# Kernel optimization log

Measured on AMD Instinct MI355X. Metric: run time of the kernel, lower is better.

Reference implementation:

```python
import jax, jax.numpy as jnp
import numpy as np

L = 2000          # per-modality dialogue length (all_dia_len)
M = 3             # num_modal
F = 512           # feature_size
E = 400000        # number of edges (<= 500000 edge_weight params)
N = M * L         # total nodes
NUM_LAYERS = 2
EW_SIZE = 500000
W_SCALE = 0.044   # ~1/sqrt(F) to keep activations sane


def setup_inputs() -> dict:
    key = jax.random.key(0)
    ks = jax.random.split(key, 9)
    x_a = jax.random.normal(ks[0], (L, F), jnp.float32)
    x_v = jax.random.normal(ks[1], (L, F), jnp.float32)
    x_t = jax.random.normal(ks[2], (L, F), jnp.float32)
    edge_index = jax.random.randint(ks[3], (2, E), 0, N, dtype=jnp.int32)
    edge_weight_param = jnp.ones((EW_SIZE,), jnp.float32)
    gcn_W = jax.random.normal(ks[4], (NUM_LAYERS, F, F), jnp.float32) * W_SCALE
    gcn_b = jnp.zeros((NUM_LAYERS, F), jnp.float32)
    fc_W = jax.random.normal(ks[5], (NUM_LAYERS, F, F), jnp.float32) * W_SCALE
    fc_b = jnp.zeros((NUM_LAYERS, F), jnp.float32)
    return {
        "x_a": x_a, "x_v": x_v, "x_t": x_t,
        "edge_weight_param": edge_weight_param,
        "gcn_W": gcn_W, "gcn_b": gcn_b,
        "fc_W": fc_W, "fc_b": fc_b,
        "edge_index": edge_index,
    }


def _gcn_fact(edge_index, edge_weight, num_nodes):
    # sparse edge list -> dense adjacency (scatter-add, duplicate edges coalesce)
    adj = jnp.zeros((num_nodes, num_nodes), edge_weight.dtype)
    adj = adj.at[edge_index[0], edge_index[1]].add(edge_weight)
    row_sum = adj.sum(axis=1)
    # torch: pow(row_sum, -0.5), inf -> 0  (safe form for zero-degree nodes)
    pos = row_sum > 0
    d_inv_sqrt = jnp.where(pos, jax.lax.rsqrt(jnp.where(pos, row_sum, 1.0)), 0.0)
    # D^{-1/2} A D^{-1/2} via row/col broadcast (same math as diag matmuls)
    return d_inv_sqrt[:, None] * adj * d_inv_sqrt[None, :]


def reference(x_a, x_v, x_t, edge_weight_param, gcn_W, gcn_b, fc_W, fc_b, edge_index):
    feature = jnp.concatenate([x_a, x_v, x_t], axis=0)      # [N, F]
    edge_weight = edge_weight_param[: edge_index.shape[1]]   # [E]
    gcn = _gcn_fact(edge_index, edge_weight, feature.shape[0])
    feature_sum = feature
    for i in range(NUM_LAYERS):
        # encoder layer: one dense GCN propagation + projection
        feature = jax.nn.relu(gcn @ feature @ gcn_W[i] + gcn_b[i])
        # fc layer: Linear + LeakyReLU (dropout = identity at eval)
        feature_sum = feature_sum + jax.nn.leaky_relu(feature @ fc_W[i] + fc_b[i], 0.01)
    # chunk back into per-modality features
    return tuple(jnp.split(feature_sum, M, axis=0))
```

## Files before the change

### kernel.cpp

```cpp
#include <hip/hip_runtime.h>
#include <hip/hip_bf16.h>

#define LL 2000
#define MM 3
#define FF 512
#define NN (MM * LL)
#define NQ 4
#define QW 1500
#define CAPQ 64

typedef __attribute__((ext_vector_type(8))) short bf16x8;
typedef __attribute__((ext_vector_type(4))) float f32x4;

__device__ __forceinline__ unsigned short f2bf(float x) {
    __hip_bfloat16 b = __float2bfloat16(x);
    return *(unsigned short*)&b;
}

__device__ __forceinline__ void gload16(const void* gsrc, void* ldst) {
    __builtin_amdgcn_global_load_lds((const __attribute__((address_space(1))) unsigned int*)gsrc,
                                     (__attribute__((address_space(3))) unsigned int*)ldst,
                                     16, 0, 0);
}

__global__ __launch_bounds__(256) void prep(const float* __restrict__ xa,
                                            const float* __restrict__ xv,
                                            const float* __restrict__ xt,
                                            unsigned short* __restrict__ feat,
                                            float* __restrict__ out_sum,
                                            const float* __restrict__ gcnW,
                                            const float* __restrict__ fcW,
                                            unsigned short* __restrict__ Wt) {
    __shared__ unsigned short tile[64][65];
    int b = blockIdx.x;
    int tid = threadIdx.x;
    if (b < 3000) {
        int idx4 = b * 256 + tid;
        const int per4 = (LL * FF) / 4;
        const float4* src;
        int off;
        if (idx4 < per4)            { src = (const float4*)xa; off = idx4; }
        else if (idx4 < 2 * per4)   { src = (const float4*)xv; off = idx4 - per4; }
        else                        { src = (const float4*)xt; off = idx4 - 2 * per4; }
        float4 v = src[off];
        ((float4*)out_sum)[idx4] = v;
        ushort4 pk;
        pk.x = f2bf(v.x); pk.y = f2bf(v.y); pk.z = f2bf(v.z); pk.w = f2bf(v.w);
        ((ushort4*)feat)[idx4] = pk;
    } else {
        int idx = b - 3000;
        int mz = idx >> 6;
        int rem = idx & 63;
        int k0 = (rem >> 3) * 64;
        int n0 = (rem & 7) * 64;
        int layer = (mz < 2) ? mz : mz - 2;
        const float* src = (mz < 2) ? (gcnW + (size_t)layer * FF * FF)
                                    : (fcW + (size_t)layer * FF * FF);
        int slot = (mz < 2) ? (mz * 2) : ((mz - 2) * 2 + 1);
        unsigned short* dst = Wt + (size_t)slot * FF * FF;
        for (int i = tid; i < 64 * 64; i += 256) {
            int r = i >> 6, c = i & 63;
            tile[r][c] = f2bf(src[(size_t)(k0 + r) * FF + n0 + c]);
        }
        __syncthreads();
        for (int i = tid; i < 64 * 64; i += 256) {
            int r = i >> 6, c = i & 63;
            dst[(size_t)(n0 + r) * FF + k0 + c] = tile[c][r];
        }
    }
}

__global__ __launch_bounds__(256) void gemm0_scatter(const unsigned short* __restrict__ A,
                                                     const unsigned short* __restrict__ Bt,
                                                     unsigned short* __restrict__ Hout,
                                                     int M, int gxm, int sblk,
                                                     const int* __restrict__ esrc,
                                                     const int* __restrict__ edst,
                                                     const float* __restrict__ ew,
                                                     int* __restrict__ counts4,
                                                     float* __restrict__ rowsumF,
                                                     unsigned int* __restrict__ bucket, int E) {
    __shared__ short As[64 * 64];
    __shared__ short Bs[64 * 64];
    int b = blockIdx.x;
    int tid = threadIdx.x;
    if (b < sblk) {
        int e = b * 256 + tid;
        if (e < E) {
            int r = esrc[e];
            int c = edst[e];
            float wv = ew[e];
            int q = c / QW;
            int slot = atomicAdd(&counts4[r * NQ + q], 1);
            if (slot < CAPQ)
                bucket[(size_t)(r * NQ + q) * CAPQ + slot] =
                    ((unsigned int)f2bf(wv) << 16) | (unsigned int)c;
            atomicAdd(&rowsumF[r], wv);
        }
        return;
    }
    int bg = b - sblk;
    int wave = tid >> 6;
    int lane = tid & 63;
    int lane16 = lane & 15;
    int quad = lane >> 4;
    int m0 = (bg % gxm) * 64;
    int n0 = (bg / gxm) * 64;
    int wm = (wave >> 1) * 32;
    int wn = (wave & 1) * 32;

    f32x4 acc[2][2] = {};

    for (int k0 = 0; k0 < FF; k0 += 64) {
#pragma unroll
        for (int s = 0; s < 2; s++) {
            int c = wave * 128 + s * 64 + lane;
            int row = c >> 3;
            int kc = (c & 7) ^ (row & 7);
            int ar = m0 + row; if (ar >= M) ar = M - 1;
            gload16((const short*)A + (size_t)ar * FF + k0 + kc * 8,
                    &As[(wave * 128 + s * 64) * 8]);
            gload16((const short*)Bt + (size_t)(n0 + row) * FF + k0 + kc * 8,
                    &Bs[(wave * 128 + s * 64) * 8]);
        }
        __syncthreads();
#pragma unroll
        for (int kk = 0; kk < 2; kk++) {
            bf16x8 a[2], bb[2];
#pragma unroll
            for (int mt = 0; mt < 2; mt++) {
                int row = wm + mt * 16 + lane16;
                int kc = (kk * 4 + quad) ^ (row & 7);
                a[mt] = *(const bf16x8*)&As[row * 64 + kc * 8];
            }
#pragma unroll
            for (int nt = 0; nt < 2; nt++) {
                int row = wn + nt * 16 + lane16;
                int kc = (kk * 4 + quad) ^ (row & 7);
                bb[nt] = *(const bf16x8*)&Bs[row * 64 + kc * 8];
            }
#pragma unroll
            for (int mt = 0; mt < 2; mt++)
#pragma unroll
                for (int nt = 0; nt < 2; nt++)
                    acc[mt][nt] = __builtin_amdgcn_mfma_f32_16x16x32_bf16(a[mt], bb[nt], acc[mt][nt], 0, 0, 0);
        }
        __syncthreads();
    }

#pragma unroll
    for (int mt = 0; mt < 2; mt++) {
#pragma unroll
        for (int nt = 0; nt < 2; nt++) {
            int n = n0 + wn + nt * 16 + lane16;
#pragma unroll
            for (int rr = 0; rr < 4; rr++) {
                int m = m0 + wm + mt * 16 + quad * 4 + rr;
                if (m < M) Hout[(size_t)m * FF + n] = f2bf(acc[mt][nt][rr]);
            }
        }
    }
}

__device__ __forceinline__ void accum8(float* acc, uint4 h, float v) {
    unsigned int d[4] = {h.x, h.y, h.z, h.w};
#pragma unroll
    for (int k = 0; k < 4; k++) {
        float lo = __uint_as_float(d[k] << 16);
        float hi = __uint_as_float(d[k] & 0xFFFF0000u);
        acc[2 * k]     = fmaf(v, lo, acc[2 * k]);
        acc[2 * k + 1] = fmaf(v, hi, acc[2 * k + 1]);
    }
}

__device__ __forceinline__ float edgev(unsigned int q, const float* __restrict__ rowsumF) {
    float rc = rowsumF[q & 0xFFFF];
    float d = (rc > 0.0f) ? rsqrtf(rc) : 0.0f;
    return __uint_as_float(q & 0xFFFF0000u) * d;
}

__global__ __launch_bounds__(256) void spmm_bias_relu(const unsigned short* __restrict__ H,
                                                      const int* __restrict__ counts4,
                                                      const unsigned int* __restrict__ bucket,
                                                      const float* __restrict__ rowsumF,
                                                      const float* __restrict__ bias,
                                                      unsigned short* __restrict__ featOut) {
    int wave = threadIdx.x >> 6, lane = threadIdx.x & 63;
    int r = blockIdx.x * 4 + wave;
    int f0 = lane * 8;
    const unsigned short* Hf = H + f0;
    float acc[8] = {0, 0, 0, 0, 0, 0, 0, 0};

#pragma unroll 1
    for (int qt = 0; qt < NQ; qt++) {
        int s = (r * NQ + qt) * CAPQ;
        int e = s + min(counts4[r * NQ + qt], CAPQ);
        int i = s;
        uint4 pk;
        bool have = (i + 4 <= e);
        if (have) pk = *(const uint4*)&bucket[i];
        while (have) {
            unsigned int q0 = pk.x, q1 = pk.y, q2 = pk.z, q3 = pk.w;
            uint4 a0 = *(const uint4*)(Hf + (size_t)(q0 & 0xFFFF) * FF);
            uint4 a1 = *(const uint4*)(Hf + (size_t)(q1 & 0xFFFF) * FF);
            uint4 a2 = *(const uint4*)(Hf + (size_t)(q2 & 0xFFFF) * FF);
            uint4 a3 = *(const uint4*)(Hf + (size_t)(q3 & 0xFFFF) * FF);
            float v0 = edgev(q0, rowsumF);
            float v1 = edgev(q1, rowsumF);
            float v2 = edgev(q2, rowsumF);
            float v3 = edgev(q3, rowsumF);
            i += 4;
            have = (i + 4 <= e);
            if (have) pk = *(const uint4*)&bucket[i];
            accum8(acc, a0, v0);
            accum8(acc, a1, v1);
            accum8(acc, a2, v2);
            accum8(acc, a3, v3);
        }
        for (; i < e; i++) {
            unsigned int q = bucket[i];
            uint4 a = *(const uint4*)(Hf + (size_t)(q & 0xFFFF) * FF);
            accum8(acc, a, edgev(q, rowsumF));
        }
    }

    float rsr = rowsumF[r];
    float dr = (rsr > 0.0f) ? rsqrtf(rsr) : 0.0f;
    float4 b0 = *(const float4*)(bias + f0);
    float4 b1 = *(const float4*)(bias + f0 + 4);
    float bb[8] = {b0.x, b0.y, b0.z, b0.w, b1.x, b1.y, b1.z, b1.w};
    unsigned int o[4];
#pragma unroll
    for (int k = 0; k < 4; k++) {
        float v0 = fmaxf(fmaf(acc[2 * k], dr, bb[2 * k]), 0.0f);
        float v1 = fmaxf(fmaf(acc[2 * k + 1], dr, bb[2 * k + 1]), 0.0f);
        o[k] = (unsigned int)f2bf(v0) | ((unsigned int)f2bf(v1) << 16);
    }
    uint4 ov; ov.x = o[0]; ov.y = o[1]; ov.z = o[2]; ov.w = o[3];
    *(uint4*)(featOut + (size_t)r * FF + f0) = ov;
}

template <int MODE>
__global__ __launch_bounds__(256) void gemm_bf16(const unsigned short* __restrict__ A,
                                                 const unsigned short* __restrict__ Bt,
                                                 const float* __restrict__ fbias,
                                                 unsigned short* __restrict__ Hout,
                                                 float* __restrict__ out,
                                                 int M) {
    __shared__ short As[64 * 64];
    __shared__ short Bs[64 * 64];
    int tid = threadIdx.x;
    int wave = tid >> 6;
    int lane = tid & 63;
    int lane16 = lane & 15;
    int quad = lane >> 4;
    int m0 = blockIdx.x * 64;
    int n0 = blockIdx.y * 64;
    int wm = (wave >> 1) * 32;
    int wn = (wave & 1) * 32;

    f32x4 acc[2][2] = {};

    for (int k0 = 0; k0 < FF; k0 += 64) {
#pragma unroll
        for (int s = 0; s < 2; s++) {
            int c = wave * 128 + s * 64 + lane;
            int row = c >> 3;
            int kc = (c & 7) ^ (row & 7);
            int ar = m0 + row; if (ar >= M) ar = M - 1;
            gload16((const short*)A + (size_t)ar * FF + k0 + kc * 8,
                    &As[(wave * 128 + s * 64) * 8]);
            gload16((const short*)Bt + (size_t)(n0 + row) * FF + k0 + kc * 8,
                    &Bs[(wave * 128 + s * 64) * 8]);
        }
        __syncthreads();
#pragma unroll
        for (int kk = 0; kk < 2; kk++) {
            bf16x8 a[2], bb[2];
#pragma unroll
            for (int mt = 0; mt < 2; mt++) {
                int row = wm + mt * 16 + lane16;
                int kc = (kk * 4 + quad) ^ (row & 7);
                a[mt] = *(const bf16x8*)&As[row * 64 + kc * 8];
            }
#pragma unroll
            for (int nt = 0; nt < 2; nt++) {
                int row = wn + nt * 16 + lane16;
                int kc = (kk * 4 + quad) ^ (row & 7);
                bb[nt] = *(const bf16x8*)&Bs[row * 64 + kc * 8];
            }
#pragma unroll
            for (int mt = 0; mt < 2; mt++)
#pragma unroll
                for (int nt = 0; nt < 2; nt++)
                    acc[mt][nt] = __builtin_amdgcn_mfma_f32_16x16x32_bf16(a[mt], bb[nt], acc[mt][nt], 0, 0, 0);
        }
        __syncthreads();
    }

    bool isFc = (MODE == 1) || (MODE == 2 && n0 < FF);
#pragma unroll
    for (int mt = 0; mt < 2; mt++) {
#pragma unroll
        for (int nt = 0; nt < 2; nt++) {
            int n = n0 + wn + nt * 16 + lane16;
            float bv = isFc ? fbias[n] : 0.0f;
#pragma unroll
            for (int rr = 0; rr < 4; rr++) {
                int m = m0 + wm + mt * 16 + quad * 4 + rr;
                if (m < M) {
                    float v = acc[mt][nt][rr];
                    if (isFc) {
                        v += bv;
                        v = (v > 0.0f) ? v : 0.01f * v;
                        out[(size_t)m * FF + n] += v;
                    } else {
                        Hout[(size_t)m * FF + (n - FF)] = f2bf(v);
                    }
                }
            }
        }
    }
}

extern "C" void kernel_launch(void* const* d_in, const int* in_sizes, int n_in,
                              void* d_out, int out_size, void* d_ws, size_t ws_size,
                              hipStream_t stream) {
    const float* xa      = (const float*)d_in[0];
    const float* xv      = (const float*)d_in[1];
    const float* xt      = (const float*)d_in[2];
    const float* ew      = (const float*)d_in[3];
    const float* gcn_W   = (const float*)d_in[4];
    const float* gcn_b   = (const float*)d_in[5];
    const float* fc_W    = (const float*)d_in[6];
    const float* fc_b    = (const float*)d_in[7];
    const int*   eidx    = (const int*)d_in[8];
    const int E = in_sizes[8] / 2;
    const int* esrc = eidx;
    const int* edst = eidx + E;

    float* out = (float*)d_out;

    char* w = (char*)d_ws;
    int*          counts4 = (int*)         (w + 0);
    float*        rowsumF = (float*)       (w + 96064);
    unsigned int* bucket  = (unsigned int*)(w + 120128);
    unsigned short* feat  = (unsigned short*)(w + 6264128);
    unsigned short* H     = (unsigned short*)(w + 12408128);
    unsigned short* Wt    = (unsigned short*)(w + 18552128);

    hipMemsetAsync(counts4, 0, 120128, stream);

    prep<<<3256, 256, 0, stream>>>(xa, xv, xt, feat, out, gcn_W, fc_W, Wt);

    const int eblocks = (E + 255) / 256;
    const int gxm = (NN + 63) / 64;
    const int ngemm0 = gxm * 8;
    gemm0_scatter<<<eblocks + ngemm0, 256, 0, stream>>>(feat, Wt, H, NN, gxm, eblocks,
                                                        esrc, edst, ew,
                                                        counts4, rowsumF, bucket, E);

    spmm_bias_relu<<<NN / 4, 256, 0, stream>>>(H, counts4, bucket, rowsumF, gcn_b, feat);
    gemm_bf16<2><<<dim3(gxm, 16), 256, 0, stream>>>(feat, Wt + (size_t)FF * FF, fc_b, H, out, NN);
    spmm_bias_relu<<<NN / 4, 256, 0, stream>>>(H, counts4, bucket, rowsumF, gcn_b + FF, feat);
    gemm_bf16<1><<<dim3(gxm, 8), 256, 0, stream>>>(feat, Wt + (size_t)3 * FF * FF, fc_b + FF, nullptr, out, NN);
}
```

Measured before the change: 244.4 us.

## Split edge bucketing into slot-count pass and precompute D^-1/2 per row

```diff
diff --git a/kernel.cpp b/kernel.cpp
--- a/kernel.cpp
+++ b/kernel.cpp
@@ -30,7 +30,11 @@
                                             float* __restrict__ out_sum,
                                             const float* __restrict__ gcnW,
                                             const float* __restrict__ fcW,
-                                            unsigned short* __restrict__ Wt) {
+                                            unsigned short* __restrict__ Wt,
+                                            const int* __restrict__ esrc,
+                                            const int* __restrict__ edst,
+                                            int* __restrict__ counts4,
+                                            int* __restrict__ pir, int E) {
     __shared__ unsigned short tile[64][65];
     int b = blockIdx.x;
     int tid = threadIdx.x;
@@ -47,7 +51,7 @@
         ushort4 pk;
         pk.x = f2bf(v.x); pk.y = f2bf(v.y); pk.z = f2bf(v.z); pk.w = f2bf(v.w);
         ((ushort4*)feat)[idx4] = pk;
-    } else {
+    } else if (b < 3256) {
         int idx = b - 3000;
         int mz = idx >> 6;
         int rem = idx & 63;
@@ -67,6 +71,12 @@
             int r = i >> 6, c = i & 63;
             dst[(size_t)(n0 + r) * FF + k0 + c] = tile[c][r];
         }
+    } else {
+        int e = (b - 3256) * 256 + tid;
+        if (e < E) {
+            int q = edst[e] / QW;
+            pir[e] = atomicAdd(&counts4[esrc[e] * NQ + q], 1);
+        }
     }
 }
 
@@ -77,8 +87,7 @@
                                                      const int* __restrict__ esrc,
                                                      const int* __restrict__ edst,
                                                      const float* __restrict__ ew,
-                                                     int* __restrict__ counts4,
-                                                     float* __restrict__ rowsumF,
+                                                     const int* __restrict__ pir,
                                                      unsigned int* __restrict__ bucket, int E) {
     __shared__ short As[64 * 64];
     __shared__ short Bs[64 * 64];
@@ -89,13 +98,11 @@
         if (e < E) {
             int r = esrc[e];
             int c = edst[e];
-            float wv = ew[e];
             int q = c / QW;
-            int slot = atomicAdd(&counts4[r * NQ + q], 1);
+            int slot = pir[e];
             if (slot < CAPQ)
                 bucket[(size_t)(r * NQ + q) * CAPQ + slot] =
-                    ((unsigned int)f2bf(wv) << 16) | (unsigned int)c;
-            atomicAdd(&rowsumF[r], wv);
+                    ((unsigned int)f2bf(ew[e]) << 16) | (unsigned int)c;
         }
         return;
     }
@@ -162,6 +169,24 @@
     }
 }
 
+__global__ __launch_bounds__(256) void rowsum_dinv(const unsigned int* __restrict__ bucket,
+                                                   const int* __restrict__ counts4,
+                                                   float* __restrict__ dinv) {
+    int wave = threadIdx.x >> 6, lane = threadIdx.x & 63;
+    int r = blockIdx.x * 4 + wave;
+    float sum = 0.0f;
+#pragma unroll
+    for (int qt = 0; qt < NQ; qt++) {
+        int s = (r * NQ + qt) * CAPQ;
+        int cnt = min(counts4[r * NQ + qt], CAPQ);
+        if (lane < cnt)
+            sum += __uint_as_float(bucket[s + lane] & 0xFFFF0000u);
+    }
+#pragma unroll
+    for (int off = 32; off > 0; off >>= 1) sum += __shfl_xor(sum, off);
+    if (lane == 0) dinv[r] = (sum > 0.0f) ? rsqrtf(sum) : 0.0f;
+}
+
 __device__ __forceinline__ void accum8(float* acc, uint4 h, float v) {
     unsigned int d[4] = {h.x, h.y, h.z, h.w};
 #pragma unroll
@@ -173,16 +198,10 @@
     }
 }
 
-__device__ __forceinline__ float edgev(unsigned int q, const float* __restrict__ rowsumF) {
-    float rc = rowsumF[q & 0xFFFF];
-    float d = (rc > 0.0f) ? rsqrtf(rc) : 0.0f;
-    return __uint_as_float(q & 0xFFFF0000u) * d;
-}
-
 __global__ __launch_bounds__(256) void spmm_bias_relu(const unsigned short* __restrict__ H,
                                                       const int* __restrict__ counts4,
                                                       const unsigned int* __restrict__ bucket,
-                                                      const float* __restrict__ rowsumF,
+                                                      const float* __restrict__ dinv,
                                                       const float* __restrict__ bias,
                                                       unsigned short* __restrict__ featOut) {
     int wave = threadIdx.x >> 6, lane = threadIdx.x & 63;
@@ -201,14 +220,14 @@
         if (have) pk = *(const uint4*)&bucket[i];
         while (have) {
             unsigned int q0 = pk.x, q1 = pk.y, q2 = pk.z, q3 = pk.w;
-            uint4 a0 = *(const uint4*)(Hf + (size_t)(q0 & 0xFFFF) * FF);
-            uint4 a1 = *(const uint4*)(Hf + (size_t)(q1 & 0xFFFF) * FF);
-            uint4 a2 = *(const uint4*)(Hf + (size_t)(q2 & 0xFFFF) * FF);
-            uint4 a3 = *(const uint4*)(Hf + (size_t)(q3 & 0xFFFF) * FF);
-            float v0 = edgev(q0, rowsumF);
-            float v1 = edgev(q1, rowsumF);
-            float v2 = edgev(q2, rowsumF);
-            float v3 = edgev(q3, rowsumF);
+            uint4 a0 = *(const uint4*)(Hf + (size_t)(q0 & 0xFFFFu) * FF);
+            uint4 a1 = *(const uint4*)(Hf + (size_t)(q1 & 0xFFFFu) * FF);
+            uint4 a2 = *(const uint4*)(Hf + (size_t)(q2 & 0xFFFFu) * FF);
+            uint4 a3 = *(const uint4*)(Hf + (size_t)(q3 & 0xFFFFu) * FF);
+            float v0 = __uint_as_float(q0 & 0xFFFF0000u) * dinv[q0 & 0xFFFFu];
+            float v1 = __uint_as_float(q1 & 0xFFFF0000u) * dinv[q1 & 0xFFFFu];
+            float v2 = __uint_as_float(q2 & 0xFFFF0000u) * dinv[q2 & 0xFFFFu];
+            float v3 = __uint_as_float(q3 & 0xFFFF0000u) * dinv[q3 & 0xFFFFu];
             i += 4;
             have = (i + 4 <= e);
             if (have) pk = *(const uint4*)&bucket[i];
@@ -219,13 +238,12 @@
         }
         for (; i < e; i++) {
             unsigned int q = bucket[i];
-            uint4 a = *(const uint4*)(Hf + (size_t)(q & 0xFFFF) * FF);
-            accum8(acc, a, edgev(q, rowsumF));
-        }
-    }
-
-    float rsr = rowsumF[r];
-    float dr = (rsr > 0.0f) ? rsqrtf(rsr) : 0.0f;
+            uint4 a = *(const uint4*)(Hf + (size_t)(q & 0xFFFFu) * FF);
+            accum8(acc, a, __uint_as_float(q & 0xFFFF0000u) * dinv[q & 0xFFFFu]);
+        }
+    }
+
+    float dr = dinv[r];
     float4 b0 = *(const float4*)(bias + f0);
     float4 b1 = *(const float4*)(bias + f0 + 4);
     float bb[8] = {b0.x, b0.y, b0.z, b0.w, b1.x, b1.y, b1.z, b1.w};
@@ -343,25 +361,28 @@
 
     char* w = (char*)d_ws;
     int*          counts4 = (int*)         (w + 0);
-    float*        rowsumF = (float*)       (w + 96064);
+    float*        dinv    = (float*)       (w + 96064);
     unsigned int* bucket  = (unsigned int*)(w + 120128);
     unsigned short* feat  = (unsigned short*)(w + 6264128);
     unsigned short* H     = (unsigned short*)(w + 12408128);
     unsigned short* Wt    = (unsigned short*)(w + 18552128);
-
-    hipMemsetAsync(counts4, 0, 120128, stream);
-
-    prep<<<3256, 256, 0, stream>>>(xa, xv, xt, feat, out, gcn_W, fc_W, Wt);
+    int*          pir     = (int*)         (w + 20649280);
+
+    hipMemsetAsync(counts4, 0, 96000, stream);
 
     const int eblocks = (E + 255) / 256;
+    prep<<<3256 + eblocks, 256, 0, stream>>>(xa, xv, xt, feat, out,
+                                             gcn_W, fc_W, Wt, esrc, edst,
+                                             counts4, pir, E);
+
     const int gxm = (NN + 63) / 64;
     const int ngemm0 = gxm * 8;
     gemm0_scatter<<<eblocks + ngemm0, 256, 0, stream>>>(feat, Wt, H, NN, gxm, eblocks,
-                                                        esrc, edst, ew,
-                                                        counts4, rowsumF, bucket, E);
-
-    spmm_bias_relu<<<NN / 4, 256, 0, stream>>>(H, counts4, bucket, rowsumF, gcn_b, feat);
+                                                        esrc, edst, ew, pir, bucket, E);
+    rowsum_dinv<<<NN / 4, 256, 0, stream>>>(bucket, counts4, dinv);
+
+    spmm_bias_relu<<<NN / 4, 256, 0, stream>>>(H, counts4, bucket, dinv, gcn_b, feat);
     gemm_bf16<2><<<dim3(gxm, 16), 256, 0, stream>>>(feat, Wt + (size_t)FF * FF, fc_b, H, out, NN);
-    spmm_bias_relu<<<NN / 4, 256, 0, stream>>>(H, counts4, bucket, rowsumF, gcn_b + FF, feat);
+    spmm_bias_relu<<<NN / 4, 256, 0, stream>>>(H, counts4, bucket, dinv, gcn_b + FF, feat);
     gemm_bf16<1><<<dim3(gxm, 8), 256, 0, stream>>>(feat, Wt + (size_t)3 * FF * FF, fc_b + FF, nullptr, out, NN);
 }
```

Measured after the change: 224.3 us. 8.2% less time.
